# Kernel tuning notes

Hardware: AMD Instinct MI355X
Metric: run time of the kernel (lower is better)

Reference implementation:

```python
import jax, jax.numpy as jnp
import numpy as np

B, S, H = 256, 196, 1024  # batch, image_size**2, hidden_size


def _linear_init(key, fan_in, fan_out):
    kw, kb = jax.random.split(key)
    lim = 1.0 / np.sqrt(fan_in)
    W = jax.random.uniform(kw, (fan_in, fan_out), jnp.float32, -lim, lim)
    b = jax.random.uniform(kb, (fan_out,), jnp.float32, -lim, lim)
    return W, b


def setup_inputs() -> dict:
    key = jax.random.key(0)
    ks = jax.random.split(key, 7)
    v = jax.random.normal(ks[0], (B, S, H), jnp.float32)
    h = jax.random.normal(ks[1], (B, H), jnp.float32)
    W_fc, b_fc = _linear_init(ks[2], H, 2 * H)
    W_v, b_v = _linear_init(ks[3], H, H)
    W_h, b_h = _linear_init(ks[4], H, H)
    W_s, b_s = _linear_init(ks[5], H, H)
    W_z, b_z = _linear_init(ks[6], H, 1)
    return {"v": v, "h": h, "W_fc": W_fc, "b_fc": b_fc, "W_v": W_v, "b_v": b_v,
            "W_h": W_h, "b_h": b_h, "W_s": W_s, "b_s": b_s, "W_z": W_z, "b_z": b_z}


def reference(v, h, W_fc, b_fc, W_v, b_v, W_h, b_h, W_s, b_s, W_z, b_z):
    # Dropout is identity in eval mode.
    hs = jnp.tanh(h[:, None, :] @ W_fc + b_fc)          # (B, 1, 2H)
    h1, s = hs[..., :H], hs[..., H:]                    # each (B, 1, H)
    _v = v @ W_v + b_v                                  # (B, S, H)
    _h = h1 @ W_h + b_h                                 # (B, 1, H)
    _s = s @ W_s + b_s                                  # (B, 1, H)
    z = jnp.tanh(jnp.concatenate([_v, _s], axis=1) + _h)  # (B, S+1, H)
    z = (z @ W_z + b_z)[..., 0]                         # (B, S+1)
    a = jax.nn.softmax(z, axis=1)                       # (B, S+1)
    vc = jnp.concatenate([v, s], axis=1)                # (B, S+1, H)
    c = jnp.sum(a[:, :, None] * vc, axis=1)             # (B, H)
    return a, c
```

## Files before the change

### kernel.cpp

```cpp
#include <hip/hip_runtime.h>
#include <hip/hip_bf16.h>
#include <cstdint>
#include <cstddef>

#define Bb  256
#define Ss  196
#define Hh  1024
#define SP1 197
#define Mm  50176

typedef float  f32x4 __attribute__((ext_vector_type(4)));
typedef short  s16x8 __attribute__((ext_vector_type(8)));
typedef unsigned short u16;
typedef unsigned short u16x4 __attribute__((ext_vector_type(4)));
typedef unsigned short u16x8 __attribute__((ext_vector_type(8)));

__device__ __forceinline__ u16 f2b(float f) {
  __hip_bfloat16 b = __float2bfloat16(f);
  u16 r; __builtin_memcpy(&r, &b, 2); return r;
}
__device__ __forceinline__ float b2f(u16 u) {
  return __uint_as_float(((unsigned)u) << 16);
}
__device__ __forceinline__ float ftanh(float x) {
  float ax = fabsf(x);
  float t = __expf(-2.f * ax);
  float r = (1.f - t) * __builtin_amdgcn_rcpf(1.f + t);
  return copysignf(r, x);
}
__device__ __forceinline__ void gload16(const u16* g, u16* l) {
  __builtin_amdgcn_global_load_lds(
      (const __attribute__((address_space(1))) unsigned int*)(const void*)g,
      (__attribute__((address_space(3))) unsigned int*)(void*)l, 16, 0, 0);
}

__device__ __forceinline__ void cvt_core(int bid, const float* __restrict__ V,
                                         u16* __restrict__ Vb) {
  const size_t total = (size_t)Mm * (Hh / 4);
  for (size_t g = (size_t)bid * 256 + threadIdx.x; g < total;
       g += (size_t)2048 * 256) {
    f32x4 a = *(const f32x4*)(V + g * 4);
    u16x4 w;
    w[0] = f2b(a.x); w[1] = f2b(a.y); w[2] = f2b(a.z); w[3] = f2b(a.w);
    *(u16x4*)(Vb + g * 4) = w;
  }
}

__device__ __forceinline__ void transpose_core(int bid, float* sm,
                                               const float* __restrict__ Wv,
                                               u16* __restrict__ WvT) {
  float (*t)[65] = (float(*)[65])sm;
  int k0 = (bid & 15) * 64;
  int n0 = (bid >> 4) * 64;
  int tid = threadIdx.x;
#pragma unroll
  for (int i = 0; i < 16; ++i) {
    int idx = i * 256 + tid;
    int r = idx >> 6, c = idx & 63;
    t[r][c] = Wv[(size_t)(k0 + r) * Hh + n0 + c];
  }
  __syncthreads();
#pragma unroll
  for (int i = 0; i < 16; ++i) {
    int idx = i * 256 + tid;
    int r = idx >> 6, c = idx & 63;
    WvT[(size_t)(n0 + r) * Hh + ((k0 + c) ^ ((r & 7) << 3))] = f2b(t[c][r]);
  }
}

__device__ __forceinline__ void small_gemm_core(int bid, int nct, float* sm,
    const float* __restrict__ X, int ldx,
    const float* __restrict__ W, int ldw,
    const float* __restrict__ bias,
    float* __restrict__ Y, int ldy, int act) {
  int tid = threadIdx.x, lane = tid & 63, w = tid >> 6;
  int ct = bid % nct, bt = bid / nct;
  int col = ct * 64 + lane;
  float acc[16];
#pragma unroll
  for (int b = 0; b < 16; ++b) acc[b] = 0.f;
  int xr = lane >> 2, xc = (lane & 3) * 16;
  for (int kc = 0; kc < 4; ++kc) {
    int kb = w * 256 + kc * 64;
#pragma unroll
    for (int q = 0; q < 4; ++q)
      *(f32x4*)&sm[(w * 16 + xr) * 64 + xc + q * 4] =
          *(const f32x4*)&X[(size_t)(bt * 16 + xr) * ldx + kb + xc + q * 4];
    for (int kl = 0; kl < 64; kl += 4) {
      float w0 = W[(size_t)(kb + kl + 0) * ldw + col];
      float w1 = W[(size_t)(kb + kl + 1) * ldw + col];
      float w2 = W[(size_t)(kb + kl + 2) * ldw + col];
      float w3 = W[(size_t)(kb + kl + 3) * ldw + col];
#pragma unroll
      for (int b = 0; b < 16; ++b) {
        f32x4 x = *(const f32x4*)&sm[(w * 16 + b) * 64 + kl];
        acc[b] += x.x * w0 + x.y * w1 + x.z * w2 + x.w * w3;
      }
    }
  }
#pragma unroll
  for (int b = 0; b < 16; ++b) sm[(w * 16 + b) * 64 + lane] = acc[b];
  __syncthreads();
#pragma unroll
  for (int q = 0; q < 4; ++q) {
    int b = w * 4 + q;
    float s = sm[(0 * 16 + b) * 64 + lane] + sm[(1 * 16 + b) * 64 + lane]
            + sm[(2 * 16 + b) * 64 + lane] + sm[(3 * 16 + b) * 64 + lane]
            + bias[col];
    if (act) s = ftanh(s);
    Y[(size_t)(bt * 16 + b) * ldy + col] = s;
  }
}

__global__ __launch_bounds__(256) void k_pre1(const float* __restrict__ v,
                                              u16* __restrict__ Vb, int pre,
                                              const float* __restrict__ Wv,
                                              u16* __restrict__ WvT,
                                              const float* __restrict__ h,
                                              const float* __restrict__ Wfc,
                                              const float* __restrict__ bfc,
                                              float* __restrict__ hs) {
  __shared__ __align__(16) float sm[64 * 65];
  int bid = blockIdx.x;
  if (bid < 256) transpose_core(bid, sm, Wv, WvT);
  else if (bid < 768)
    small_gemm_core(bid - 256, 32, sm, h, Hh, Wfc, 2048, bfc, hs, 2048, 1);
  else if (pre) cvt_core(bid - 768, v, Vb);
}

__global__ __launch_bounds__(256) void k_dual(const float* __restrict__ hs,
                                              const float* __restrict__ Wh,
                                              const float* __restrict__ bh,
                                              const float* __restrict__ Ws_,
                                              const float* __restrict__ bs_,
                                              float* __restrict__ hhp,
                                              float* __restrict__ svp) {
  __shared__ __align__(16) float sm[4 * 16 * 64];
  int bid = blockIdx.x;
  int sel = bid >= 256;
  small_gemm_core(bid - (sel << 8), 16, sm,
                  sel ? hs + 1024 : hs, 2048,
                  sel ? Ws_ : Wh, Hh,
                  sel ? bs_ : bh,
                  sel ? svp : hhp, Hh, 0);
}

#define BK 64
template<int PRE>
__global__ __launch_bounds__(256, PRE ? 4 : 3)
void k_big(const float* __restrict__ V, const u16* __restrict__ Vb,
           const u16* __restrict__ WvT, const float* __restrict__ bv,
           const float* __restrict__ hh, const float* __restrict__ Wz,
           float* __restrict__ zpart) {
  constexpr int LDA_ = PRE ? 64 : 72;
  __shared__ __align__(16) u16 As[128 * LDA_];
  __shared__ __align__(16) u16 Bs[128 * 64];
  __shared__ float wz_s[128], bv_s[128], hh_s[2][128];
  __shared__ float zred[4][64];

  int bid = blockIdx.x;
  int lin = (bid & 7) * 392 + (bid >> 3);
  int mt = lin >> 3, nt = lin & 7;
  int row0 = mt * 128, n0 = nt * 128;

  int tid = threadIdx.x;
  int lane = tid & 63, wid = tid >> 6;
  int wm = wid >> 1, wn = wid & 1;

  int b0 = row0 / Ss;
  int rsplit = (b0 + 1) * Ss - row0;
  int b1 = (rsplit < 128) ? b0 + 1 : b0;
  if (tid < 128) {
    wz_s[tid] = Wz[n0 + tid];
    bv_s[tid] = bv[n0 + tid];
    hh_s[0][tid] = hh[(size_t)b0 * Hh + n0 + tid];
    hh_s[1][tid] = hh[(size_t)b1 * Hh + n0 + tid];
  }

  f32x4 acc[4][4];
  f32x4 zz = {0.f, 0.f, 0.f, 0.f};
#pragma unroll
  for (int m = 0; m < 4; ++m)
#pragma unroll
    for (int n = 0; n < 4; ++n) acc[m][n] = zz;

  int srow = lane >> 3, scol = (lane & 7) * 8;
  int ascol = scol ^ (srow << 3);
  int bxor = (lane & 7) << 3;

  int arow = tid >> 3, acol8 = (tid & 7) * 8;
  const float* Ap = V + (size_t)(row0 + arow) * Hh + acol8;
  f32x4 av[8];
  if constexpr (!PRE) {
#pragma unroll
    for (int j = 0; j < 4; ++j) {
      av[2 * j]     = *(const f32x4*)(Ap + (size_t)j * 32 * Hh);
      av[2 * j + 1] = *(const f32x4*)(Ap + (size_t)j * 32 * Hh + 4);
    }
  }

  for (int kt = 0; kt < 16; ++kt) {
    int k0 = kt * BK;
    __syncthreads();
    if constexpr (PRE) {
#pragma unroll
      for (int i = 0; i < 4; ++i) {
        int r = wid * 32 + i * 8;
        gload16(WvT + (size_t)(n0 + r + srow) * Hh + k0 + scol, &Bs[r * 64]);
      }
#pragma unroll
      for (int i = 0; i < 4; ++i) {
        int r = wid * 32 + i * 8;
        gload16(Vb + (size_t)(row0 + r + srow) * Hh + k0 + ascol, &As[r * 64]);
      }
    } else {
#pragma unroll
      for (int i = 0; i < 4; ++i) {
        int r = wid * 32 + i * 8;
        gload16(WvT + (size_t)(n0 + r + srow) * Hh + k0 + scol, &Bs[r * 64]);
      }
#pragma unroll
      for (int j = 0; j < 4; ++j) {
        u16x8 w;
        w[0] = f2b(av[2 * j].x);     w[1] = f2b(av[2 * j].y);
        w[2] = f2b(av[2 * j].z);     w[3] = f2b(av[2 * j].w);
        w[4] = f2b(av[2 * j + 1].x); w[5] = f2b(av[2 * j + 1].y);
        w[6] = f2b(av[2 * j + 1].z); w[7] = f2b(av[2 * j + 1].w);
        *(u16x8*)&As[(j * 32 + arow) * LDA_ + acol8] = w;
      }
      if (kt < 15) {
#pragma unroll
        for (int j = 0; j < 4; ++j) {
          av[2 * j]     = *(const f32x4*)(Ap + (size_t)j * 32 * Hh + k0 + BK);
          av[2 * j + 1] = *(const f32x4*)(Ap + (size_t)j * 32 * Hh + k0 + BK + 4);
        }
      }
    }
    __syncthreads();
#pragma unroll
    for (int ks = 0; ks < 2; ++ks) {
      int kk = ks * 32 + (lane >> 4) * 8;
      s16x8 afr[4], bfr[4];
#pragma unroll
      for (int m = 0; m < 4; ++m) {
        int r = wm * 64 + m * 16 + (lane & 15);
        afr[m] = *(const s16x8*)&As[r * LDA_ + (PRE ? (kk ^ bxor) : kk)];
      }
#pragma unroll
      for (int n = 0; n < 4; ++n) {
        int r = wn * 64 + n * 16 + (lane & 15);
        bfr[n] = *(const s16x8*)&Bs[r * 64 + (kk ^ bxor)];
      }
#pragma unroll
      for (int m = 0; m < 4; ++m)
#pragma unroll
        for (int n = 0; n < 4; ++n)
          acc[m][n] = __builtin_amdgcn_mfma_f32_16x16x32_bf16(afr[m], bfr[n], acc[m][n], 0, 0, 0);
    }
  }

  int cl = lane & 15, rg = lane >> 4;
  float pz[4][4];
#pragma unroll
  for (int m = 0; m < 4; ++m)
#pragma unroll
    for (int j = 0; j < 4; ++j) pz[m][j] = 0.f;
#pragma unroll
  for (int n = 0; n < 4; ++n) {
    int col = wn * 64 + n * 16 + cl;
    float wzv = wz_s[col], bvv = bv_s[col];
    float h0 = hh_s[0][col], h1 = hh_s[1][col];
#pragma unroll
    for (int m = 0; m < 4; ++m)
#pragma unroll
      for (int j = 0; j < 4; ++j) {
        int r = wm * 64 + m * 16 + rg * 4 + j;
        float hv = (r >= rsplit) ? h1 : h0;
        pz[m][j] += wzv * ftanh(acc[m][n][j] + bvv + hv);
      }
  }
#pragma unroll
  for (int m = 0; m < 4; ++m)
#pragma unroll
    for (int j = 0; j < 4; ++j) {
      float vv = pz[m][j];
      vv += __shfl_xor(vv, 1); vv += __shfl_xor(vv, 2);
      vv += __shfl_xor(vv, 4); vv += __shfl_xor(vv, 8);
      pz[m][j] = vv;
    }
  if (cl == 0) {
#pragma unroll
    for (int m = 0; m < 4; ++m)
#pragma unroll
      for (int j = 0; j < 4; ++j)
        zred[wid][m * 16 + rg * 4 + j] = pz[m][j];
  }
  __syncthreads();
  if (tid < 128) {
    int hhalf = tid >> 6, lr = tid & 63;
    zpart[(size_t)nt * Mm + row0 + tid] =
        zred[hhalf * 2][lr] + zred[hhalf * 2 + 1][lr];
  }
}

__global__ __launch_bounds__(256) void k_softmax(const float* __restrict__ zpart,
                                                 const float* __restrict__ sv,
                                                 const float* __restrict__ hhp,
                                                 const float* __restrict__ Wz,
                                                 const float* __restrict__ bz,
                                                 float* __restrict__ outA) {
  int b = blockIdx.x, tid = threadIdx.x;
  int wid = tid >> 6, lane = tid & 63;
  __shared__ float redm[4], reds[4];
  __shared__ float zSsh;
  {
    int j0 = tid * 4;
    f32x4 s4 = *(const f32x4*)&sv[(size_t)b * Hh + j0];
    f32x4 h4 = *(const f32x4*)&hhp[(size_t)b * Hh + j0];
    f32x4 w4 = *(const f32x4*)&Wz[j0];
    float p = w4.x * ftanh(s4.x + h4.x) + w4.y * ftanh(s4.y + h4.y)
            + w4.z * ftanh(s4.z + h4.z) + w4.w * ftanh(s4.w + h4.w);
#pragma unroll
    for (int d = 1; d < 64; d <<= 1) p += __shfl_xor(p, d);
    if (lane == 0) redm[wid] = p;
    __syncthreads();
    if (tid == 0) zSsh = redm[0] + redm[1] + redm[2] + redm[3] + bz[0];
    __syncthreads();
  }
  float z = -1e30f;
  if (tid < Ss) {
    float s = 0.f;
#pragma unroll
    for (int nt = 0; nt < 8; ++nt) s += zpart[(size_t)nt * Mm + (size_t)b * Ss + tid];
    z = s + bz[0];
  } else if (tid == Ss) {
    z = zSsh;
  }
  float m = z;
#pragma unroll
  for (int d = 1; d < 64; d <<= 1) m = fmaxf(m, __shfl_xor(m, d));
  if (lane == 0) redm[wid] = m;
  __syncthreads();
  m = fmaxf(fmaxf(redm[0], redm[1]), fmaxf(redm[2], redm[3]));
  float e = (tid <= Ss) ? expf(z - m) : 0.f;
  float s = e;
#pragma unroll
  for (int d = 1; d < 64; d <<= 1) s += __shfl_xor(s, d);
  if (lane == 0) reds[wid] = s;
  __syncthreads();
  s = reds[0] + reds[1] + reds[2] + reds[3];
  if (tid <= Ss) outA[(size_t)b * SP1 + tid] = e / s;
}

template<int PRE>
__global__ __launch_bounds__(256) void k_ctx(const float* __restrict__ V,
                                             const u16* __restrict__ Vb,
                                             const float* __restrict__ hs,
                                             const float* __restrict__ A,
                                             float* __restrict__ outC) {
  __shared__ float a_s[SP1];
  if constexpr (PRE) {
    int b = blockIdx.x;
    int c4 = threadIdx.x * 4;
    if (threadIdx.x < SP1) a_s[threadIdx.x] = A[(size_t)b * SP1 + threadIdx.x];
    __syncthreads();
    f32x4 hv = *(const f32x4*)&hs[(size_t)b * 2048 + 1024 + c4];
    float aS = a_s[Ss];
    f32x4 acc = {aS * hv.x, aS * hv.y, aS * hv.z, aS * hv.w};
    const u16* vb = Vb + (size_t)b * Ss * Hh + c4;
#pragma unroll 4
    for (int t = 0; t < Ss; ++t) {
      u16x4 w = *(const u16x4*)(vb + (size_t)t * Hh);
      float at = a_s[t];
      acc.x += at * b2f(w[0]); acc.y += at * b2f(w[1]);
      acc.z += at * b2f(w[2]); acc.w += at * b2f(w[3]);
    }
    *(f32x4*)&outC[(size_t)b * Hh + c4] = acc;
  } else {
    int b = blockIdx.x >> 2;
    int col = (blockIdx.x & 3) * 256 + threadIdx.x;
    if (threadIdx.x < SP1) a_s[threadIdx.x] = A[(size_t)b * SP1 + threadIdx.x];
    __syncthreads();
    float acc = a_s[Ss] * hs[(size_t)b * 2048 + 1024 + col];
    const float* vb = V + (size_t)b * Ss * Hh + col;
#pragma unroll 4
    for (int t = 0; t < Ss; ++t) acc += a_s[t] * vb[(size_t)t * Hh];
    outC[(size_t)b * Hh + col] = acc;
  }
}

extern "C" void kernel_launch(void* const* d_in, const int* in_sizes, int n_in,
                              void* d_out, int out_size, void* d_ws, size_t ws_size,
                              hipStream_t stream) {
  const float* v   = (const float*)d_in[0];
  const float* h   = (const float*)d_in[1];
  const float* Wfc = (const float*)d_in[2];
  const float* bfc = (const float*)d_in[3];
  const float* Wv  = (const float*)d_in[4];
  const float* bv  = (const float*)d_in[5];
  const float* Wh  = (const float*)d_in[6];
  const float* bh  = (const float*)d_in[7];
  const float* Ws  = (const float*)d_in[8];
  const float* bs  = (const float*)d_in[9];
  const float* Wz  = (const float*)d_in[10];
  const float* bz  = (const float*)d_in[11];
  float* out  = (float*)d_out;
  float* outA = out;
  float* outC = out + (size_t)Bb * SP1;

  float* ws  = (float*)d_ws;
  float* hs  = ws;
  float* hh  = hs + 524288;
  float* sv  = hh + 262144;
  float* zp  = sv + 262144;
  u16*  WvT  = (u16*)(zp + 401408);
  u16*  Vb   = (u16*)((char*)(void*)WvT + 2097152);

  bool pre = ws_size >= 110657536ull;

  k_pre1<<<2816, 256, 0, stream>>>(v, Vb, (int)pre, Wv, WvT, h, Wfc, bfc, hs);
  k_dual<<<512, 256, 0, stream>>>(hs, Wh, bh, Ws, bs, hh, sv);
  if (pre) k_big<1><<<3136, 256, 0, stream>>>(v, Vb, WvT, bv, hh, Wz, zp);
  else     k_big<0><<<3136, 256, 0, stream>>>(v, Vb, WvT, bv, hh, Wz, zp);
  k_softmax<<<256, 256, 0, stream>>>(zp, sv, hh, Wz, bz, outA);
  if (pre) k_ctx<1><<<256, 256, 0, stream>>>(v, Vb, hs, outA, outC);
  else     k_ctx<0><<<1024, 256, 0, stream>>>(v, Vb, hs, outA, outC);
}
```

Baseline: 271.3 us.

## Add 256x256-tile 8-wave GEMM kernel with double-buffered LDS and interleaved loads

Adds k_big8, which computes the V·Wv GEMM with 256x256 output tiles on 512 threads. It double-buffers A/B in LDS and interleaves global loads with quadrant-wise MFMA phases behind explicit barriers, using setprio around the MFMAs. Larger tiles raise arithmetic intensity and halve the N-partial count from 8 to 4, so softmax now takes the partial count as a parameter. Costs include heavier register pressure (128 accumulator floats per thread), 128KB+ of LDS per block, and a fragile hand-written vmcnt schedule.

```diff
diff --git a/kernel.cpp b/kernel.cpp
--- a/kernel.cpp
+++ b/kernel.cpp
@@ -145,6 +145,195 @@
                   sel ? svp : hhp, Hh, 0);
 }
 
+__device__ __forceinline__ void rdA8(const u16* __restrict__ buf, int base_row,
+                                     int hi8, int kxor, s16x8 (&afr)[4][2]) {
+#pragma unroll
+  for (int m = 0; m < 4; ++m)
+#pragma unroll
+    for (int ks = 0; ks < 2; ++ks)
+      afr[m][ks] = *(const s16x8*)&buf[(base_row + m * 16) * 64 + ((ks * 32 + hi8) ^ kxor)];
+}
+__device__ __forceinline__ void rdB8(const u16* __restrict__ buf, int base_row,
+                                     int hi8, int kxor, s16x8 (&bfr)[2][2]) {
+#pragma unroll
+  for (int n = 0; n < 2; ++n)
+#pragma unroll
+    for (int ks = 0; ks < 2; ++ks)
+      bfr[n][ks] = *(const s16x8*)&buf[(base_row + n * 16) * 64 + ((ks * 32 + hi8) ^ kxor)];
+}
+template<int MQ, int NQ>
+__device__ __forceinline__ void mmaQ(f32x4 (&acc)[8][4], const s16x8 (&afr)[4][2],
+                                     const s16x8 (&bfr)[2][2]) {
+  __builtin_amdgcn_s_setprio(1);
+#pragma unroll
+  for (int m = 0; m < 4; ++m)
+#pragma unroll
+    for (int n = 0; n < 2; ++n)
+#pragma unroll
+      for (int ks = 0; ks < 2; ++ks)
+        acc[MQ * 4 + m][NQ * 2 + n] = __builtin_amdgcn_mfma_f32_16x16x32_bf16(
+            afr[m][ks], bfr[n][ks], acc[MQ * 4 + m][NQ * 2 + n], 0, 0, 0);
+  __builtin_amdgcn_s_setprio(0);
+}
+__device__ __forceinline__ void st_half8(const u16* __restrict__ gbase, int grow0,
+                                         int hf, int wid, int srow, int colofs,
+                                         int t, u16* __restrict__ dst) {
+#pragma unroll
+  for (int j = 0; j < 2; ++j) {
+    int r = hf * 128 + (wid * 2 + j) * 8;
+    gload16(gbase + (size_t)(grow0 + r + srow) * Hh + t * 64 + colofs, dst + r * 64);
+  }
+}
+#define BAR_MID() do { __builtin_amdgcn_s_barrier(); \
+  asm volatile("s_waitcnt lgkmcnt(0)" ::: "memory"); \
+  __builtin_amdgcn_sched_barrier(0); } while (0)
+#define BAR_END() do { __builtin_amdgcn_s_barrier(); \
+  __builtin_amdgcn_sched_barrier(0); } while (0)
+
+__global__ __launch_bounds__(512, 2)
+void k_big8(const u16* __restrict__ Vb, const u16* __restrict__ WvT,
+            const float* __restrict__ bv, const float* __restrict__ hh,
+            const float* __restrict__ Wz, float* __restrict__ zpart) {
+  __shared__ __align__(16) u16 As0[256 * 64], As1[256 * 64];
+  __shared__ __align__(16) u16 Bs0[256 * 64], Bs1[256 * 64];
+  __shared__ float zred[4][256];
+
+  int bid = blockIdx.x;
+  int lin = (bid & 7) * 98 + (bid >> 3);
+  int mt = lin >> 2, nt = lin & 3;
+  int row0 = mt * 256, n0 = nt * 256;
+
+  int tid = threadIdx.x;
+  int lane = tid & 63, wid = tid >> 6;
+  int wm = wid >> 2, wn = wid & 3;
+  int l15 = lane & 15, rg = lane >> 4;
+  int srow = lane >> 3, scol = (lane & 7) * 8;
+  int ascol = scol ^ (srow << 3);
+  int kxor = (lane & 7) << 3;
+  int hi8 = rg * 8;
+  int arowA0 = wm * 128 + l15;
+  int arowA1 = wm * 128 + 64 + l15;
+  int browB0 = wn * 64 + l15;
+  int browB1 = wn * 64 + 32 + l15;
+
+  f32x4 acc[8][4];
+  f32x4 zz = {0.f, 0.f, 0.f, 0.f};
+#pragma unroll
+  for (int m = 0; m < 8; ++m)
+#pragma unroll
+    for (int n = 0; n < 4; ++n) acc[m][n] = zz;
+  s16x8 afr0[4][2], afr1[4][2], bfr0[2][2], bfr1[2][2];
+
+  st_half8(Vb, row0, 0, wid, srow, ascol, 0, As0);
+  st_half8(Vb, row0, 1, wid, srow, ascol, 0, As0);
+  st_half8(WvT, n0, 0, wid, srow, scol, 0, Bs0);
+  st_half8(WvT, n0, 1, wid, srow, scol, 0, Bs0);
+  st_half8(WvT, n0, 0, wid, srow, scol, 1, Bs1);
+  st_half8(Vb, row0, 0, wid, srow, ascol, 1, As1);
+  st_half8(Vb, row0, 1, wid, srow, ascol, 1, As1);
+  asm volatile("s_waitcnt vmcnt(6)" ::: "memory");
+  __builtin_amdgcn_s_barrier();
+  __builtin_amdgcn_sched_barrier(0);
+
+#pragma unroll 1
+  for (int it = 0; it < 8; ++it) {
+    int t1 = 2 * it + 1, t2 = 2 * it + 2, t3 = 2 * it + 3;
+    bool nf = (it < 7);
+    rdA8(As0, arowA0, hi8, kxor, afr0);
+    rdB8(Bs0, browB0, hi8, kxor, bfr0);
+    st_half8(WvT, n0, 1, wid, srow, scol, t1, Bs1);
+    BAR_MID();
+    mmaQ<0, 0>(acc, afr0, bfr0);
+    BAR_END();
+    rdA8(As0, arowA1, hi8, kxor, afr1);
+    rdB8(Bs0, browB1, hi8, kxor, bfr1);
+    if (nf) st_half8(WvT, n0, 0, wid, srow, scol, t2, Bs0);
+    BAR_MID();
+    mmaQ<1, 1>(acc, afr1, bfr1);
+    BAR_END();
+    if (nf) st_half8(Vb, row0, 0, wid, srow, ascol, t2, As0);
+    BAR_MID();
+    mmaQ<1, 0>(acc, afr1, bfr0);
+    BAR_END();
+    if (nf) st_half8(Vb, row0, 1, wid, srow, ascol, t2, As0);
+    BAR_MID();
+    mmaQ<0, 1>(acc, afr0, bfr1);
+    if (nf) asm volatile("s_waitcnt vmcnt(6)" ::: "memory");
+    else    asm volatile("s_waitcnt vmcnt(0)" ::: "memory");
+    __builtin_amdgcn_s_barrier();
+    __builtin_amdgcn_sched_barrier(0);
+    rdA8(As1, arowA0, hi8, kxor, afr0);
+    rdB8(Bs1, browB0, hi8, kxor, bfr0);
+    if (nf) st_half8(WvT, n0, 1, wid, srow, scol, t2, Bs0);
+    BAR_MID();
+    mmaQ<0, 0>(acc, afr0, bfr0);
+    BAR_END();
+    rdA8(As1, arowA1, hi8, kxor, afr1);
+    rdB8(Bs1, browB1, hi8, kxor, bfr1);
+    if (nf) st_half8(WvT, n0, 0, wid, srow, scol, t3, Bs1);
+    BAR_MID();
+    mmaQ<1, 1>(acc, afr1, bfr1);
+    BAR_END();
+    if (nf) st_half8(Vb, row0, 0, wid, srow, ascol, t3, As1);
+    BAR_MID();
+    mmaQ<1, 0>(acc, afr1, bfr0);
+    BAR_END();
+    if (nf) st_half8(Vb, row0, 1, wid, srow, ascol, t3, As1);
+    BAR_MID();
+    mmaQ<0, 1>(acc, afr0, bfr1);
+    if (nf) asm volatile("s_waitcnt vmcnt(6)" ::: "memory");
+    __builtin_amdgcn_s_barrier();
+    __builtin_amdgcn_sched_barrier(0);
+  }
+
+  int b0 = row0 / Ss;
+  int rs1 = (b0 + 1) * Ss - row0;
+  int rs2 = rs1 + Ss;
+  int b1 = (b0 + 1 < Bb) ? b0 + 1 : b0;
+  int b2 = (b0 + 2 < Bb) ? b0 + 2 : b1;
+  float pz[8][4];
+#pragma unroll
+  for (int im = 0; im < 8; ++im)
+#pragma unroll
+    for (int j = 0; j < 4; ++j) pz[im][j] = 0.f;
+#pragma unroll
+  for (int in = 0; in < 4; ++in) {
+    int col = n0 + wn * 64 + in * 16 + l15;
+    float wzv = Wz[col], bvv = bv[col];
+    float h0 = hh[(size_t)b0 * Hh + col];
+    float h1 = hh[(size_t)b1 * Hh + col];
+    float h2 = hh[(size_t)b2 * Hh + col];
+#pragma unroll
+    for (int im = 0; im < 8; ++im)
+#pragma unroll
+      for (int j = 0; j < 4; ++j) {
+        int r = wm * 128 + im * 16 + rg * 4 + j;
+        float hv = (r >= rs2) ? h2 : ((r >= rs1) ? h1 : h0);
+        pz[im][j] += wzv * ftanh(acc[im][in][j] + bvv + hv);
+      }
+  }
+#pragma unroll
+  for (int im = 0; im < 8; ++im)
+#pragma unroll
+    for (int j = 0; j < 4; ++j) {
+      float vv = pz[im][j];
+      vv += __shfl_xor(vv, 1); vv += __shfl_xor(vv, 2);
+      vv += __shfl_xor(vv, 4); vv += __shfl_xor(vv, 8);
+      pz[im][j] = vv;
+    }
+  if (l15 == 0) {
+#pragma unroll
+    for (int im = 0; im < 8; ++im)
+#pragma unroll
+      for (int j = 0; j < 4; ++j)
+        zred[wn][wm * 128 + im * 16 + rg * 4 + j] = pz[im][j];
+  }
+  __syncthreads();
+  if (tid < 256)
+    zpart[(size_t)nt * Mm + row0 + tid] =
+        zred[0][tid] + zred[1][tid] + zred[2][tid] + zred[3][tid];
+}
+
 #define BK 64
 template<int PRE>
 __global__ __launch_bounds__(256, PRE ? 4 : 3)
@@ -304,6 +493,7 @@
 }
 
 __global__ __launch_bounds__(256) void k_softmax(const float* __restrict__ zpart,
+                                                 int np,
                                                  const float* __restrict__ sv,
                                                  const float* __restrict__ hhp,
                                                  const float* __restrict__ Wz,
@@ -330,8 +520,8 @@
   float z = -1e30f;
   if (tid < Ss) {
     float s = 0.f;
-#pragma unroll
-    for (int nt = 0; nt < 8; ++nt) s += zpart[(size_t)nt * Mm + (size_t)b * Ss + tid];
+    for (int ntp = 0; ntp < np; ++ntp)
+      s += zpart[(size_t)ntp * Mm + (size_t)b * Ss + tid];
     z = s + bz[0];
   } else if (tid == Ss) {
     z = zSsh;
@@ -420,9 +610,13 @@
 
   k_pre1<<<2816, 256, 0, stream>>>(v, Vb, (int)pre, Wv, WvT, h, Wfc, bfc, hs);
   k_dual<<<512, 256, 0, stream>>>(hs, Wh, bh, Ws, bs, hh, sv);
-  if (pre) k_big<1><<<3136, 256, 0, stream>>>(v, Vb, WvT, bv, hh, Wz, zp);
-  else     k_big<0><<<3136, 256, 0, stream>>>(v, Vb, WvT, bv, hh, Wz, zp);
-  k_softmax<<<256, 256, 0, stream>>>(zp, sv, hh, Wz, bz, outA);
-  if (pre) k_ctx<1><<<256, 256, 0, stream>>>(v, Vb, hs, outA, outC);
-  else     k_ctx<0><<<1024, 256, 0, stream>>>(v, Vb, hs, outA, outC);
-}
+  if (pre) {
+    k_big8<<<784, 512, 0, stream>>>(Vb, WvT, bv, hh, Wz, zp);
+    k_softmax<<<256, 256, 0, stream>>>(zp, 4, sv, hh, Wz, bz, outA);
+    k_ctx<1><<<256, 256, 0, stream>>>(v, Vb, hs, outA, outC);
+  } else {
+    k_big<0><<<3136, 256, 0, stream>>>(v, Vb, WvT, bv, hh, Wz, zp);
+    k_softmax<<<256, 256, 0, stream>>>(zp, 8, sv, hh, Wz, bz, outA);
+    k_ctx<0><<<1024, 256, 0, stream>>>(v, Vb, hs, outA, outC);
+  }
+}
```

After: 351.8 us. 1.3x slower.
